# Optimization experiments

Hardware: AMD Instinct MI355X
Metric: run time of the kernel (lower is better)

## Reference

```python
import jax, jax.numpy as jnp
import numpy as np


def setup_inputs() -> dict:
    key = jax.random.key(0)
    k1, k2, k3 = jax.random.split(key, 3)
    N, M, D, C = 4096, 8192, 1024, 128
    x = jax.random.normal(k1, (N, D), dtype=jnp.float32)
    x_n = jax.random.normal(k2, (M, D), dtype=jnp.float32)
    y = jax.random.uniform(k3, (M, C), dtype=jnp.float32)
    # module parameter: log_T = log(init_temperature) = log(1.0) = 0.0
    log_T = jnp.array(0.0, dtype=jnp.float32)
    return {"x": x, "x_n": x_n, "y": y, "log_T": log_T}


def reference(x, x_n, y, log_T):
    # Faithful to NONA.forward with similarity='euclidean', batch_norm=None,
    # agg=None, and x != x_n (plain softmax branch, no diagonal mask).
    T = jnp.exp(log_T)  # computed in the original forward but never applied
    del T
    # sim = -cdist(x, x_n, p=2)  via the ||a-b||^2 = ||a||^2 + ||b||^2 - 2ab expansion
    x_sq = jnp.sum(x * x, axis=1, keepdims=True)          # [N, 1]
    xn_sq = jnp.sum(x_n * x_n, axis=1)                    # [M]
    d2 = x_sq + xn_sq[None, :] - 2.0 * (x @ x_n.T)        # [N, M]
    sim = -jnp.sqrt(jnp.maximum(d2, 0.0))                 # [N, M]
    sim_scores = jax.nn.softmax(sim, axis=1)              # [N, M]
    return sim_scores @ y                                 # [N, C]
```

## Files before the change

kernel.cpp:

```cpp
#include <hip/hip_runtime.h>


#define N_ 4096
#define M_ 8192
#define D_ 1024
#define C_ 128
#define SPLIT 16
#define MCOLS (M_ / SPLIT)
#define NBN (MCOLS / 128)
#define NKK (D_ / 64)

typedef __bf16 bf16;
typedef __attribute__((ext_vector_type(8))) __bf16 bf16x8;
typedef __attribute__((ext_vector_type(4))) __bf16 bf16x4;
typedef __attribute__((ext_vector_type(4))) float f32x4;

__device__ __forceinline__ void async_copy16(const bf16* gp, void* lp) {
  __builtin_amdgcn_global_load_lds(
      (__attribute__((address_space(1))) void*)const_cast<bf16*>(gp),
      (__attribute__((address_space(3))) void*)lp, 16, 0, 0);
}

__device__ __forceinline__ int swz(int row, int gran) {
  return (row << 7) + ((gran ^ (row & 7)) << 4);
}
__device__ __forceinline__ int swz2(int row, int gran) {
  return (row << 8) + ((gran ^ (row & 15)) << 4);
}

__device__ __forceinline__ void stage16(const bf16* src, char* lds, int tid) {
  const int lane = tid & 63, wave = tid >> 6;
#pragma unroll
  for (int j = 0; j < 4; ++j) {
    const int ch  = j * 4 + wave;
    const int off = ch * 1024 + lane * 16;
    const int row = off >> 7;
    const int gr  = ((off >> 4) & 7) ^ (row & 7);
    async_copy16(src + (size_t)row * D_ + gr * 8, lds + ch * 1024);
  }
}
__device__ __forceinline__ void stageV(const bf16* yT, int colbase, char* lds, int tid) {
  const int lane = tid & 63, wave = tid >> 6;
#pragma unroll
  for (int j = 0; j < 8; ++j) {
    const int ch  = j * 4 + wave;
    const int off = ch * 1024 + lane * 16;
    const int row = off >> 8;
    const int gr  = ((off >> 4) & 15) ^ (row & 15);
    async_copy16(yT + (size_t)row * M_ + colbase + gr * 8, lds + ch * 1024);
  }
}

#define VM8 asm volatile("s_waitcnt vmcnt(8)" ::: "memory")
#define VM0 asm volatile("s_waitcnt vmcnt(0)" ::: "memory")

__global__ __launch_bounds__(256, 2)
void nona_main(const bf16* __restrict__ xb, const bf16* __restrict__ xnb,
               const bf16* __restrict__ yT, const float* __restrict__ xsq,
               const float* __restrict__ xnsq, float* __restrict__ Opart,
               float* __restrict__ Lpart)
{
  __shared__ __align__(16) char Lds[65536];
  char* const A0 = Lds;
  char* const A1 = Lds + 16384;
  char* const B0 = Lds + 32768;
  char* const B1 = Lds + 49152;
  char* const Pb = A0;
  char* const Vb = B0;

  const int tid  = threadIdx.x;
  const int lane = tid & 63;
  const int wave = tid >> 6;
  const int wr = wave >> 1, wc = wave & 1;
  const int g = lane >> 4, c = lane & 15;

  const int xcd = blockIdx.x & 7;
  const int idx = blockIdx.x >> 3;
  const int rb  = ((xcd >> 2) << 4) | (idx >> 2);
  const int s   = ((xcd & 3) << 2) | (idx & 3);
  const int row0 = rb * 128;
  const int col0 = s * MCOLS;

  const bf16* xA = xb + (size_t)row0 * D_;

  float xs[4];
#pragma unroll
  for (int rf = 0; rf < 4; ++rf)
    xs[rf] = xsq[row0 + wr * 64 + rf * 16 + c];

  f32x4 Oacc[4][4];
  const f32x4 zero = {0.f, 0.f, 0.f, 0.f};
#pragma unroll
  for (int rf = 0; rf < 4; ++rf)
#pragma unroll
    for (int cc = 0; cc < 4; ++cc) Oacc[rf][cc] = zero;
  float lsum[4] = {0.f, 0.f, 0.f, 0.f};

#pragma unroll 1
  for (int bn = 0; bn < NBN; ++bn) {
    const int colbase = col0 + bn * 128;
    const bf16* xB = xnb + (size_t)colbase * D_;

    f32x4 Sacc[4][4];
#pragma unroll
    for (int rf = 0; rf < 4; ++rf)
#pragma unroll
      for (int cf = 0; cf < 4; ++cf) Sacc[rf][cf] = zero;

    stage16(xA, A0, tid);
    stage16(xB, B0, tid);

#pragma unroll 1
    for (int kk = 0; kk < NKK; ++kk) {
      if (kk < NKK - 1) {
        stage16(xA + (kk + 1) * 64, (kk & 1) ? A0 : A1, tid);
        stage16(xB + (kk + 1) * 64, (kk & 1) ? B0 : B1, tid);
        VM8;
      } else {
        VM0;
      }
      __builtin_amdgcn_s_barrier();
      __builtin_amdgcn_sched_barrier(0);
      const char* Ac = (kk & 1) ? A1 : A0;
      const char* Bc = (kk & 1) ? B1 : B0;
#pragma unroll
      for (int ks = 0; ks < 2; ++ks) {
        bf16x8 af[4], bv[4];
#pragma unroll
        for (int rf = 0; rf < 4; ++rf)
          af[rf] = *(const bf16x8*)(Ac + swz(wr * 64 + rf * 16 + c, ks * 4 + g));
#pragma unroll
        for (int j = 0; j < 4; ++j)
          bv[j] = *(const bf16x8*)(Bc + swz(wc * 64 + j * 16 + c, ks * 4 + g));
        __builtin_amdgcn_s_setprio(1);
#pragma unroll
        for (int j = 0; j < 4; ++j)
#pragma unroll
          for (int rf = 0; rf < 4; ++rf)
            Sacc[rf][j] = __builtin_amdgcn_mfma_f32_16x16x32_bf16(
                bv[j], af[rf], Sacc[rf][j], 0, 0, 0);
        __builtin_amdgcn_s_setprio(0);
      }
      __builtin_amdgcn_sched_barrier(0);
      __builtin_amdgcn_s_barrier();
    }
    __syncthreads();

    stageV(yT, colbase, Vb, tid);

#pragma unroll
    for (int cf = 0; cf < 4; ++cf) {
      const float4 nsq4 = *(const float4*)(xnsq + colbase + wc * 64 + cf * 16 + g * 4);
#pragma unroll
      for (int rf = 0; rf < 4; ++rf)
#pragma unroll
        for (int r = 0; r < 4; ++r) {
          float d2 = xs[rf] + ((const float*)&nsq4)[r] - 2.0f * Sacc[rf][cf][r];
          d2 = fmaxf(d2, 0.0f);
          const float wv = __expf(-sqrtf(d2));
          lsum[rf] += wv;
          Sacc[rf][cf][r] = wv;
        }
    }

#pragma unroll
    for (int rf = 0; rf < 4; ++rf)
#pragma unroll
      for (int cf = 0; cf < 4; ++cf) {
        bf16x4 pk;
#pragma unroll
        for (int r = 0; r < 4; ++r) pk[r] = (bf16)Sacc[rf][cf][r];
        const int prow = wr * 64 + rf * 16 + c;
        const int gran = wc * 8 + cf * 2 + (g >> 1);
        *(bf16x4*)(Pb + (prow << 8) + ((gran ^ (prow & 15)) << 4) + (g & 1) * 8) = pk;
      }
    __syncthreads();

#pragma unroll
    for (int ks = 0; ks < 4; ++ks) {
      bf16x8 pa[4], vb[4];
#pragma unroll
      for (int rf = 0; rf < 4; ++rf)
        pa[rf] = *(const bf16x8*)(Pb + swz2(wr * 64 + rf * 16 + c, ks * 4 + g));
#pragma unroll
      for (int cc = 0; cc < 4; ++cc)
        vb[cc] = *(const bf16x8*)(Vb + swz2(wc * 64 + cc * 16 + c, ks * 4 + g));
      __builtin_amdgcn_s_setprio(1);
#pragma unroll
      for (int cc = 0; cc < 4; ++cc)
#pragma unroll
        for (int rf = 0; rf < 4; ++rf)
          Oacc[rf][cc] = __builtin_amdgcn_mfma_f32_16x16x32_bf16(pa[rf], vb[cc], Oacc[rf][cc], 0, 0, 0);
      __builtin_amdgcn_s_setprio(0);
    }
    __syncthreads();
  }

  float* Lr = (float*)Lds;
#pragma unroll
  for (int rf = 0; rf < 4; ++rf) {
    float v = lsum[rf];
    v += __shfl_xor(v, 16);
    v += __shfl_xor(v, 32);
    if (g == 0) Lr[wc * 128 + wr * 64 + rf * 16 + c] = v;
  }
  __syncthreads();
  if (tid < 128)
    Lpart[(size_t)s * N_ + row0 + tid] = Lr[tid] + Lr[128 + tid];

  float* ob = Opart + ((size_t)s * N_ + row0) * C_;
#pragma unroll
  for (int rf = 0; rf < 4; ++rf)
#pragma unroll
    for (int cc = 0; cc < 4; ++cc)
#pragma unroll
      for (int r = 0; r < 4; ++r)
        ob[(wr * 64 + rf * 16 + g * 4 + r) * C_ + wc * 64 + cc * 16 + c] = Oacc[rf][cc][r];
}

__global__ void prep_rows(const float* __restrict__ x, const float* __restrict__ xn,
                          bf16* __restrict__ xb, bf16* __restrict__ xnb,
                          float* __restrict__ xsq, float* __restrict__ xnsq)
{
  const int blk = blockIdx.x;
  const float* src; bf16* dst; float* sq; int row;
  if (blk < N_) { src = x;  dst = xb;  sq = xsq;  row = blk; }
  else          { src = xn; dst = xnb; sq = xnsq; row = blk - N_; }
  const int t = threadIdx.x;
  const float4 v = reinterpret_cast<const float4*>(src + (size_t)row * D_)[t];
  float ss = v.x * v.x + v.y * v.y + v.z * v.z + v.w * v.w;
  bf16x4 hv;
  hv[0] = (bf16)v.x; hv[1] = (bf16)v.y; hv[2] = (bf16)v.z; hv[3] = (bf16)v.w;
  *reinterpret_cast<bf16x4*>(dst + (size_t)row * D_ + t * 4) = hv;
#pragma unroll
  for (int o = 32; o > 0; o >>= 1) ss += __shfl_down(ss, o);
  __shared__ float red[4];
  if ((t & 63) == 0) red[t >> 6] = ss;
  __syncthreads();
  if (t == 0) sq[row] = red[0] + red[1] + red[2] + red[3];
}

__global__ void prep_yT(const float* __restrict__ y, bf16* __restrict__ yT)
{
  __shared__ bf16 tile[C_][72];
  const int m0 = blockIdx.x * 64;
  const int t = threadIdx.x;
#pragma unroll
  for (int i = 0; i < 32; ++i) {
    const int idx = i * 256 + t;
    const int ml = idx >> 7, cc = idx & 127;
    tile[cc][ml] = (bf16)y[(size_t)(m0 + ml) * C_ + cc];
  }
  __syncthreads();
#pragma unroll
  for (int i = 0; i < 32; ++i) {
    const int idx = i * 256 + t;
    const int cc = idx >> 6, ml = idx & 63;
    yT[(size_t)cc * M_ + m0 + ml] = tile[cc][ml];
  }
}

__global__ void combine(const float* __restrict__ Opart, const float* __restrict__ Lpart,
                        float* __restrict__ out)
{
  const int i = blockIdx.x * 256 + threadIdx.x;
  const int row = i >> 7;
  float o = 0.f, l = 0.f;
#pragma unroll
  for (int s = 0; s < SPLIT; ++s) {
    o += Opart[(size_t)s * N_ * C_ + i];
    l += Lpart[(size_t)s * N_ + row];
  }
  out[i] = o / l;
}

extern "C" void kernel_launch(void* const* d_in, const int* in_sizes, int n_in,
                              void* d_out, int out_size, void* d_ws, size_t ws_size,
                              hipStream_t stream)
{
  const float* x  = (const float*)d_in[0];
  const float* xn = (const float*)d_in[1];
  const float* y  = (const float*)d_in[2];
  float* out = (float*)d_out;

  char* ws = (char*)d_ws;
  bf16*  xb    = (bf16*)(ws);
  bf16*  xnb   = (bf16*)(ws + (size_t)8  * 1024 * 1024);
  bf16*  yT    = (bf16*)(ws + (size_t)24 * 1024 * 1024);
  float* xsq   = (float*)(ws + (size_t)26 * 1024 * 1024);
  float* xnsq  = (float*)(ws + (size_t)26 * 1024 * 1024 + 16 * 1024);
  float* Lpart = (float*)(ws + (size_t)26 * 1024 * 1024 + 64 * 1024);
  float* Opart = (float*)(ws + (size_t)27 * 1024 * 1024);

  prep_rows<<<N_ + M_, 256, 0, stream>>>(x, xn, xb, xnb, xsq, xnsq);
  prep_yT<<<M_ / 64, 256, 0, stream>>>(y, yT);
  nona_main<<<32 * SPLIT, 256, 0, stream>>>(xb, xnb, yT, xsq, xnsq, Opart, Lpart);
  combine<<<(N_ * C_) / 256, 256, 0, stream>>>(Opart, Lpart, out);
}
```

Before: 123.5 us.

## Load A operand fragments directly from global into registers, stage only B in LDS

The A (x row-block) tile is no longer staged through LDS. Each lane loads its MFMA A fragments straight from global memory into double-buffered registers (afA/afB), prefetching the next k-step. Only the x_n tile still goes through async global-to-LDS copies, which halves LDS traffic and LDS footprint, and the k-loop is unrolled by two to ping-pong the register and LDS buffers. The cost is more VGPRs, uncoalesced global reads of A that depend on the cache because A is reused across column blocks, and a full vmcnt(0) wait each step in place of the earlier partial wait.

After: 236.1 us. 1.91x slower.

```diff
diff --git a/kernel.cpp b/kernel.cpp
--- a/kernel.cpp
+++ b/kernel.cpp
@@ -51,8 +51,37 @@
   }
 }
 
-#define VM8 asm volatile("s_waitcnt vmcnt(8)" ::: "memory")
 #define VM0 asm volatile("s_waitcnt vmcnt(0)" ::: "memory")
+
+#define KSTEP(afc, afn, Bc, Bn, KK, DOSTG)                                     \
+  VM0;                                                                         \
+  __builtin_amdgcn_s_barrier();                                                \
+  __builtin_amdgcn_sched_barrier(0);                                           \
+  {                                                                            \
+    bf16x8 bv[4];                                                              \
+    _Pragma("unroll") for (int j = 0; j < 4; ++j)                              \
+      bv[j] = *(const bf16x8*)((Bc) + swz(wc * 64 + j * 16 + c, g));           \
+    if (DOSTG) {                                                               \
+      stage16(xB + ((KK) + 1) * 64, (Bn), tid);                                \
+      _Pragma("unroll") for (int rf = 0; rf < 4; ++rf)                         \
+      _Pragma("unroll") for (int ks = 0; ks < 2; ++ks)                         \
+        afn[rf][ks] = *(const bf16x8*)(arowg[rf] + ((KK) + 1) * 64 + ks * 32); \
+    }                                                                          \
+    __builtin_amdgcn_s_setprio(1);                                             \
+    _Pragma("unroll") for (int j = 0; j < 4; ++j)                              \
+    _Pragma("unroll") for (int rf = 0; rf < 4; ++rf)                           \
+      Sacc[rf][j] = __builtin_amdgcn_mfma_f32_16x16x32_bf16(                   \
+          bv[j], afc[rf][0], Sacc[rf][j], 0, 0, 0);                            \
+    __builtin_amdgcn_s_setprio(0);                                             \
+    _Pragma("unroll") for (int j = 0; j < 4; ++j)                              \
+      bv[j] = *(const bf16x8*)((Bc) + swz(wc * 64 + j * 16 + c, 4 + g));       \
+    __builtin_amdgcn_s_setprio(1);                                             \
+    _Pragma("unroll") for (int j = 0; j < 4; ++j)                              \
+    _Pragma("unroll") for (int rf = 0; rf < 4; ++rf)                           \
+      Sacc[rf][j] = __builtin_amdgcn_mfma_f32_16x16x32_bf16(                   \
+          bv[j], afc[rf][1], Sacc[rf][j], 0, 0, 0);                            \
+    __builtin_amdgcn_s_setprio(0);                                             \
+  }
 
 __global__ __launch_bounds__(256, 2)
 void nona_main(const bf16* __restrict__ xb, const bf16* __restrict__ xnb,
@@ -61,12 +90,10 @@
                float* __restrict__ Lpart)
 {
   __shared__ __align__(16) char Lds[65536];
-  char* const A0 = Lds;
-  char* const A1 = Lds + 16384;
-  char* const B0 = Lds + 32768;
-  char* const B1 = Lds + 49152;
-  char* const Pb = A0;
-  char* const Vb = B0;
+  char* const B0 = Lds;
+  char* const B1 = Lds + 16384;
+  char* const Vb = Lds + 32768;
+  char* const Pb = B0;
 
   const int tid  = threadIdx.x;
   const int lane = tid & 63;
@@ -82,6 +109,10 @@
   const int col0 = s * MCOLS;
 
   const bf16* xA = xb + (size_t)row0 * D_;
+  const bf16* arowg[4];
+#pragma unroll
+  for (int rf = 0; rf < 4; ++rf)
+    arowg[rf] = xA + (size_t)(wr * 64 + rf * 16 + c) * D_ + g * 8;
 
   float xs[4];
 #pragma unroll
@@ -107,42 +138,18 @@
 #pragma unroll
       for (int cf = 0; cf < 4; ++cf) Sacc[rf][cf] = zero;
 
-    stage16(xA, A0, tid);
+    bf16x8 afA[4][2], afB[4][2];
     stage16(xB, B0, tid);
+#pragma unroll
+    for (int rf = 0; rf < 4; ++rf)
+#pragma unroll
+      for (int ks = 0; ks < 2; ++ks)
+        afA[rf][ks] = *(const bf16x8*)(arowg[rf] + ks * 32);
 
 #pragma unroll 1
-    for (int kk = 0; kk < NKK; ++kk) {
-      if (kk < NKK - 1) {
-        stage16(xA + (kk + 1) * 64, (kk & 1) ? A0 : A1, tid);
-        stage16(xB + (kk + 1) * 64, (kk & 1) ? B0 : B1, tid);
-        VM8;
-      } else {
-        VM0;
-      }
-      __builtin_amdgcn_s_barrier();
-      __builtin_amdgcn_sched_barrier(0);
-      const char* Ac = (kk & 1) ? A1 : A0;
-      const char* Bc = (kk & 1) ? B1 : B0;
-#pragma unroll
-      for (int ks = 0; ks < 2; ++ks) {
-        bf16x8 af[4], bv[4];
-#pragma unroll
-        for (int rf = 0; rf < 4; ++rf)
-          af[rf] = *(const bf16x8*)(Ac + swz(wr * 64 + rf * 16 + c, ks * 4 + g));
-#pragma unroll
-        for (int j = 0; j < 4; ++j)
-          bv[j] = *(const bf16x8*)(Bc + swz(wc * 64 + j * 16 + c, ks * 4 + g));
-        __builtin_amdgcn_s_setprio(1);
-#pragma unroll
-        for (int j = 0; j < 4; ++j)
-#pragma unroll
-          for (int rf = 0; rf < 4; ++rf)
-            Sacc[rf][j] = __builtin_amdgcn_mfma_f32_16x16x32_bf16(
-                bv[j], af[rf], Sacc[rf][j], 0, 0, 0);
-        __builtin_amdgcn_s_setprio(0);
-      }
-      __builtin_amdgcn_sched_barrier(0);
-      __builtin_amdgcn_s_barrier();
+    for (int t = 0; t < 8; ++t) {
+      KSTEP(afA, afB, B0, B1, 2 * t, 1)
+      KSTEP(afB, afA, B1, B0, 2 * t + 1, (2 * t + 1) < NKK - 1)
     }
     __syncthreads();
 
```
